# Performance work log

Measured on AMD Instinct MI355X. Metric: run time of the kernel, lower is better.

The kernel has to match this reference:

```python
import jax, jax.numpy as jnp
import numpy as np

B, H, L, E, MODES = 32, 8, 4096, 64, 64


def setup_inputs() -> dict:
    key = jax.random.key(0)
    kx, kw, ki = jax.random.split(key, 3)
    x = jax.random.normal(kx, (B, H, L, E), dtype=jnp.float32)
    # nn.Parameter(torch.randn(E, E, modes, 2) / sqrt(E))
    weights = jax.random.normal(kw, (E, E, MODES, 2), dtype=jnp.float32) / np.sqrt(E)
    # register_buffer: sorted random permutation of [0, seq_len//2) truncated to modes (unique)
    index = jnp.sort(jax.random.permutation(ki, L // 2)[:MODES]).astype(jnp.int64)
    return {"x": x, "weights": weights, "index": index}


def reference(x, weights, index):
    # x: [B, H, L, E]
    Bs, Hs, Ls, Es = x.shape
    xt = jnp.swapaxes(x, -1, -2)                 # [B, H, E, L]
    x_ft = jnp.fft.rfft(xt, axis=-1)             # [B, H, E, L//2+1] complex64
    w_c = weights[..., 0] + 1j * weights[..., 1]  # [E, E, modes] complex
    sel = x_ft[..., index]                       # gather selected modes: [B, H, E, modes]
    out_sel = jnp.einsum('bhei,eoi->bhoi', sel, w_c)  # [B, H, E_out, modes]
    out_ft = jnp.zeros_like(x_ft).at[..., index].set(out_sel)  # scatter into zero spectrum
    y = jnp.fft.irfft(out_ft, n=Ls, axis=-1)     # [B, H, E, L]
    return jnp.swapaxes(y, -1, -2)               # [B, H, L, E]
```

## Files before the change

kernel.cpp:

```cpp
#include <hip/hip_runtime.h>
#include <hip/hip_bf16.h>
#include <math.h>

#define LTOT   4096
#define EDIM   64
#define NMODES 64
#define BH     256
#define TWO_PI 6.28318530717958647692f

typedef float f32x4 __attribute__((ext_vector_type(4)));
typedef short s16x8 __attribute__((ext_vector_type(8)));

__device__ inline unsigned short f2bf(float f) {
    unsigned u = __builtin_bit_cast(unsigned, f);
    u += 0x7fff + ((u >> 16) & 1);
    return (unsigned short)(u >> 16);
}
__device__ inline unsigned packbf(float lo, float hi) {
    float2 t; t.x = lo; t.y = hi;
    __hip_bfloat162 h = __float22bfloat162_rn(t);
    unsigned r;
    __builtin_memcpy(&r, &h, 4);
    return r;
}
__device__ inline float bf2f(unsigned lo16) {
    return __builtin_bit_cast(float, lo16 << 16);
}

__global__ __launch_bounds__(256) void k_tables(const int* __restrict__ index,
                                                const float* __restrict__ w,
                                                unsigned short* __restrict__ Tm,
                                                unsigned short* __restrict__ Tt,
                                                unsigned* __restrict__ wt) {
    int b = blockIdx.x, t = threadIdx.x;
    if (b < 64) {
        int k = b, f = index[k];
        for (int l = t; l < LTOT; l += 256) {
            int m = (f * l) & (LTOT - 1);
            float th = (float)m * (TWO_PI / (float)LTOT);
            float s, c; sincosf(th, &s, &c);
            Tm[(size_t)(2 * k) * LTOT + l]     = f2bf(c);
            Tm[(size_t)(2 * k + 1) * LTOT + l] = f2bf(-s);
        }
    } else if (b < 64 + 1024) {
        int l = (b - 64) * 4 + (t >> 6);
        int k = t & 63, f = index[k];
        int m = (f * l) & (LTOT - 1);
        float th = (float)m * (TWO_PI / (float)LTOT);
        float s, c; sincosf(th, &s, &c);
        ((unsigned*)Tt)[l * 64 + k] = packbf(c, s);
    } else {
        int i = (b - 1088) * 256 + t;
        float2 v = ((const float2*)w)[i];
        wt[i] = packbf(v.x, v.y);
    }
}

__global__ __launch_bounds__(256, 5) void k_stage1(const float* __restrict__ x,
                                                   const unsigned short* __restrict__ Tm,
                                                   float* __restrict__ Xp) {
    int bh = blockIdx.x >> 2, part = blockIdx.x & 3;
    const float* xb = x + ((size_t)bh * LTOT + part * 1024) * EDIM;
    __shared__ unsigned xT[64 * 68];

    int t = threadIdx.x;
    int q = t & 15, lp0 = t >> 4;
    int lane = t & 63, w = t >> 6;
    int r = lane & 15, kb8 = lane >> 4;
    int es = w & 1, ms = w >> 1;
    unsigned swzW = ((unsigned)(q & 7)) << 2;

    f32x4 acc[2][4];
    #pragma unroll
    for (int i = 0; i < 2; ++i)
        #pragma unroll
        for (int n = 0; n < 4; ++n) acc[i][n] = (f32x4)0.f;

    float4 xn[8];
    {
        #pragma unroll
        for (int p = 0; p < 4; ++p) {
            const float* bp = xb + (size_t)(2 * (lp0 + p * 16)) * EDIM + 4 * q;
            xn[2 * p]     = *(const float4*)bp;
            xn[2 * p + 1] = *(const float4*)(bp + EDIM);
        }
    }
    for (int t8 = 0; t8 < 8; ++t8) {
        #pragma unroll
        for (int p = 0; p < 4; ++p) {
            float A0[4] = {xn[2*p].x, xn[2*p].y, xn[2*p].z, xn[2*p].w};
            float A1[4] = {xn[2*p+1].x, xn[2*p+1].y, xn[2*p+1].z, xn[2*p+1].w};
            #pragma unroll
            for (int j = 0; j < 4; ++j)
                xT[(4 * q + j) * 68 + (((unsigned)(lp0 + p * 16)) ^ swzW)] = packbf(A0[j], A1[j]);
        }
        __syncthreads();
        if (t8 < 7) {
            const float* tb = xb + (size_t)((t8 + 1) * 128) * EDIM;
            #pragma unroll
            for (int p = 0; p < 4; ++p) {
                const float* bp = tb + (size_t)(2 * (lp0 + p * 16)) * EDIM + 4 * q;
                xn[2 * p]     = *(const float4*)bp;
                xn[2 * p + 1] = *(const float4*)(bp + EDIM);
            }
        }
        #pragma unroll
        for (int kk = 0; kk < 4; ++kk) {
            s16x8 af[2];
            #pragma unroll
            for (int sub = 0; sub < 2; ++sub) {
                int row = es * 32 + sub * 16 + r;
                unsigned swz = (((unsigned)sub) << 4) + (((unsigned)(r >> 2)) << 2);
                af[sub] = *(const s16x8*)(xT + row * 68 + (((unsigned)(kk * 16 + kb8 * 4)) ^ swz));
            }
            #pragma unroll
            for (int ns = 0; ns < 4; ++ns) {
                int m = ms * 64 + ns * 16 + r;
                s16x8 bf = *(const s16x8*)(Tm + (size_t)m * LTOT + part * 1024 + t8 * 128 + kk * 32 + kb8 * 8);
                acc[0][ns] = __builtin_amdgcn_mfma_f32_16x16x32_bf16(af[0], bf, acc[0][ns], 0, 0, 0);
                acc[1][ns] = __builtin_amdgcn_mfma_f32_16x16x32_bf16(af[1], bf, acc[1][ns], 0, 0, 0);
            }
        }
        __syncthreads();
    }

    float* Xb = Xp + ((size_t)part * BH + bh) * (64 * 128);
    #pragma unroll
    for (int sub = 0; sub < 2; ++sub)
        #pragma unroll
        for (int ns = 0; ns < 4; ++ns)
            #pragma unroll
            for (int g = 0; g < 4; ++g)
                Xb[(es * 32 + sub * 16 + kb8 * 4 + g) * 128 + ms * 64 + ns * 16 + r] = acc[sub][ns][g];
}

__global__ __launch_bounds__(512) void k_stage2(const float* __restrict__ Xp,
                                                const unsigned* __restrict__ wtab,
                                                const int* __restrict__ index,
                                                unsigned* __restrict__ ABo) {
    int bh = blockIdx.x;
    __shared__ float XsR[64 * 68];
    __shared__ float XsI[64 * 68];
    int t = threadIdx.x;

    #pragma unroll
    for (int i = 0; i < 4; ++i) {
        int idx = t + i * 512;
        f32x4 v = (f32x4)0.f;
        #pragma unroll
        for (int p = 0; p < 4; ++p)
            v += ((const f32x4*)(Xp + ((size_t)p * BH + bh) * 8192))[idx];
        int e = idx >> 5, k0 = (idx & 31) * 2;
        XsR[e * 68 + k0]     = v.x;
        XsI[e * 68 + k0]     = v.y;
        XsR[e * 68 + k0 + 1] = v.z;
        XsI[e * 68 + k0 + 1] = v.w;
    }
    __syncthreads();

    int k = t & 63, og = t >> 6;
    int f = index[k];
    float cc = (f == 0 ? 1.0f : 2.0f) / (float)LTOT;
    int o0 = og * 8;
    float aR[8] = {}, aI[8] = {};
    for (int e = 0; e < 64; ++e) {
        float xr = XsR[e * 68 + k];
        float xi = XsI[e * 68 + k];
        #pragma unroll
        for (int oi = 0; oi < 8; ++oi) {
            unsigned wv = wtab[((size_t)(e * 64 + o0 + oi)) * 64 + k];
            float wr = bf2f(wv & 0xffffu);
            float wi = bf2f(wv >> 16);
            aR[oi] += xr * wr - xi * wi;
            aI[oi] += xr * wi + xi * wr;
        }
    }
    #pragma unroll
    for (int oi = 0; oi < 8; ++oi) {
        float im = (f == 0) ? 0.0f : -cc * aI[oi];
        ABo[((size_t)bh * 64 + o0 + oi) * 64 + k] = packbf(cc * aR[oi], im);
    }
}

#define S3P16 136
__global__ __launch_bounds__(256, 4) void k_stage3(const unsigned short* __restrict__ Tt,
                                                   const unsigned* __restrict__ ABo,
                                                   float* __restrict__ y) {
    int bh = blockIdx.x >> 2, qtr = blockIdx.x & 3;
    __shared__ unsigned short ABl[64 * S3P16];
    int t = threadIdx.x;
    int lane = t & 63, wave = t >> 6;
    int r = lane & 15, kb8 = lane >> 4;

    {
        const unsigned* src = ABo + (size_t)bh * 4096;
        unsigned* dst = (unsigned*)ABl;
        #pragma unroll
        for (int i = 0; i < 16; ++i) {
            int idx = t + i * 256;
            int o = idx >> 6, c = idx & 63;
            dst[o * (S3P16 / 2) + c] = src[idx];
        }
    }
    __syncthreads();

    s16x8 afr[4][4];
    #pragma unroll
    for (int es = 0; es < 4; ++es)
        #pragma unroll
        for (int ks = 0; ks < 4; ++ks)
            afr[es][ks] = *(const s16x8*)(ABl + (es * 16 + r) * S3P16 + ks * 32 + kb8 * 8);

    for (int it = 0; it < 16; ++it) {
        int ltile = qtr * 1024 + it * 64 + wave * 16;
        s16x8 btf[4];
        #pragma unroll
        for (int ks = 0; ks < 4; ++ks)
            btf[ks] = *(const s16x8*)(Tt + (size_t)(ltile + r) * 128 + ks * 32 + kb8 * 8);
        f32x4 acc[4];
        #pragma unroll
        for (int es = 0; es < 4; ++es) acc[es] = (f32x4)0.f;
        #pragma unroll
        for (int ks = 0; ks < 4; ++ks)
            #pragma unroll
            for (int es = 0; es < 4; ++es)
                acc[es] = __builtin_amdgcn_mfma_f32_16x16x32_bf16(afr[es][ks], btf[ks], acc[es], 0, 0, 0);
        float* yb = y + ((size_t)bh * LTOT + ltile + r) * EDIM;
        #pragma unroll
        for (int es = 0; es < 4; ++es)
            *(f32x4*)(yb + es * 16 + kb8 * 4) = acc[es];
    }
}

extern "C" void kernel_launch(void* const* d_in, const int* in_sizes, int n_in,
                              void* d_out, int out_size, void* d_ws, size_t ws_size,
                              hipStream_t stream) {
    const float* x     = (const float*)d_in[0];
    const float* wgt   = (const float*)d_in[1];
    const int*   index = (const int*)d_in[2];
    float* y  = (float*)d_out;
    float* ws = (float*)d_ws;

    unsigned short* Tm = (unsigned short*)ws;
    unsigned short* Tt = (unsigned short*)(ws + 262144);
    unsigned*       wt = (unsigned*)(ws + 524288);
    float*          Xp = ws + 786432;
    unsigned*       ABo = (unsigned*)(ws + 9175040);

    hipLaunchKernelGGL(k_tables, dim3(2112),   dim3(256), 0, stream, index, wgt, Tm, Tt, wt);
    hipLaunchKernelGGL(k_stage1, dim3(BH * 4), dim3(256), 0, stream, x, Tm, Xp);
    hipLaunchKernelGGL(k_stage2, dim3(BH),     dim3(512), 0, stream, Xp, wt, index, ABo);
    hipLaunchKernelGGL(k_stage3, dim3(BH * 4), dim3(256), 0, stream, Tt, ABo, y);
}
```

Measured before the change: 226.2 us.

## Store stage-1 partial spectra as bf16, transpose weight table, widen stage 2

```diff
diff --git a/kernel.cpp b/kernel.cpp
--- a/kernel.cpp
+++ b/kernel.cpp
@@ -31,34 +31,38 @@
                                                 const float* __restrict__ w,
                                                 unsigned short* __restrict__ Tm,
                                                 unsigned short* __restrict__ Tt,
-                                                unsigned* __restrict__ wt) {
+                                                unsigned* __restrict__ wt2) {
     int b = blockIdx.x, t = threadIdx.x;
-    if (b < 64) {
-        int k = b, f = index[k];
-        for (int l = t; l < LTOT; l += 256) {
+    if (b < 256) {
+        int k = b >> 2, f = index[k];
+        int lq = b & 3;
+        #pragma unroll
+        for (int i = 0; i < 4; ++i) {
+            int l = lq * 1024 + i * 256 + t;
             int m = (f * l) & (LTOT - 1);
             float th = (float)m * (TWO_PI / (float)LTOT);
             float s, c; sincosf(th, &s, &c);
             Tm[(size_t)(2 * k) * LTOT + l]     = f2bf(c);
             Tm[(size_t)(2 * k + 1) * LTOT + l] = f2bf(-s);
         }
-    } else if (b < 64 + 1024) {
-        int l = (b - 64) * 4 + (t >> 6);
+    } else if (b < 256 + 1024) {
+        int l = (b - 256) * 4 + (t >> 6);
         int k = t & 63, f = index[k];
         int m = (f * l) & (LTOT - 1);
         float th = (float)m * (TWO_PI / (float)LTOT);
         float s, c; sincosf(th, &s, &c);
         ((unsigned*)Tt)[l * 64 + k] = packbf(c, s);
     } else {
-        int i = (b - 1088) * 256 + t;
+        int i = (b - 1280) * 256 + t;
+        int e = i >> 12, o = (i >> 6) & 63, k = i & 63;
         float2 v = ((const float2*)w)[i];
-        wt[i] = packbf(v.x, v.y);
+        wt2[((size_t)(e * 64 + k)) * 64 + o] = packbf(v.x, v.y);
     }
 }
 
 __global__ __launch_bounds__(256, 5) void k_stage1(const float* __restrict__ x,
                                                    const unsigned short* __restrict__ Tm,
-                                                   float* __restrict__ Xp) {
+                                                   unsigned* __restrict__ XpB) {
     int bh = blockIdx.x >> 2, part = blockIdx.x & 3;
     const float* xb = x + ((size_t)bh * LTOT + part * 1024) * EDIM;
     __shared__ unsigned xT[64 * 68];
@@ -124,20 +128,24 @@
         __syncthreads();
     }
 
-    float* Xb = Xp + ((size_t)part * BH + bh) * (64 * 128);
+    unsigned* Xb = XpB + ((size_t)part * BH + bh) * (128 * 32);
     #pragma unroll
     for (int sub = 0; sub < 2; ++sub)
         #pragma unroll
-        for (int ns = 0; ns < 4; ++ns)
-            #pragma unroll
-            for (int g = 0; g < 4; ++g)
-                Xb[(es * 32 + sub * 16 + kb8 * 4 + g) * 128 + ms * 64 + ns * 16 + r] = acc[sub][ns][g];
-}
-
-__global__ __launch_bounds__(512) void k_stage2(const float* __restrict__ Xp,
-                                                const unsigned* __restrict__ wtab,
-                                                const int* __restrict__ index,
-                                                unsigned* __restrict__ ABo) {
+        for (int ns = 0; ns < 4; ++ns) {
+            int m   = ms * 64 + ns * 16 + r;
+            int eu0 = es * 16 + sub * 8 + kb8 * 2;
+            uint2 pv;
+            pv.x = packbf(acc[sub][ns][0], acc[sub][ns][1]);
+            pv.y = packbf(acc[sub][ns][2], acc[sub][ns][3]);
+            *(uint2*)(Xb + m * 32 + eu0) = pv;
+        }
+}
+
+__global__ __launch_bounds__(1024) void k_stage2(const unsigned* __restrict__ XpB,
+                                                 const unsigned* __restrict__ wt2,
+                                                 const int* __restrict__ index,
+                                                 unsigned* __restrict__ ABo) {
     int bh = blockIdx.x;
     __shared__ float XsR[64 * 68];
     __shared__ float XsI[64 * 68];
@@ -145,38 +153,43 @@
 
     #pragma unroll
     for (int i = 0; i < 4; ++i) {
-        int idx = t + i * 512;
-        f32x4 v = (f32x4)0.f;
-        #pragma unroll
-        for (int p = 0; p < 4; ++p)
-            v += ((const f32x4*)(Xp + ((size_t)p * BH + bh) * 8192))[idx];
-        int e = idx >> 5, k0 = (idx & 31) * 2;
-        XsR[e * 68 + k0]     = v.x;
-        XsI[e * 68 + k0]     = v.y;
-        XsR[e * 68 + k0 + 1] = v.z;
-        XsI[e * 68 + k0 + 1] = v.w;
+        int idx = t + i * 1024;
+        float lo = 0.f, hi = 0.f;
+        #pragma unroll
+        for (int p = 0; p < 4; ++p) {
+            unsigned v = XpB[((size_t)p * BH + bh) * 4096 + idx];
+            lo += bf2f(v & 0xffffu);
+            hi += bf2f(v >> 16);
+        }
+        int m = idx >> 5, eu = idx & 31;
+        float* plane = (m & 1) ? XsI : XsR;
+        int k = m >> 1;
+        plane[(2 * eu) * 68 + k]     = lo;
+        plane[(2 * eu + 1) * 68 + k] = hi;
     }
     __syncthreads();
 
     int k = t & 63, og = t >> 6;
     int f = index[k];
     float cc = (f == 0 ? 1.0f : 2.0f) / (float)LTOT;
-    int o0 = og * 8;
-    float aR[8] = {}, aI[8] = {};
+    int o0 = og * 4;
+    float aR[4] = {}, aI[4] = {};
+    #pragma unroll 4
     for (int e = 0; e < 64; ++e) {
         float xr = XsR[e * 68 + k];
         float xi = XsI[e * 68 + k];
-        #pragma unroll
-        for (int oi = 0; oi < 8; ++oi) {
-            unsigned wv = wtab[((size_t)(e * 64 + o0 + oi)) * 64 + k];
-            float wr = bf2f(wv & 0xffffu);
-            float wi = bf2f(wv >> 16);
+        uint4 wv = *(const uint4*)&wt2[((size_t)(e * 64 + k)) * 64 + o0];
+        unsigned wa[4] = {wv.x, wv.y, wv.z, wv.w};
+        #pragma unroll
+        for (int oi = 0; oi < 4; ++oi) {
+            float wr = bf2f(wa[oi] & 0xffffu);
+            float wi = bf2f(wa[oi] >> 16);
             aR[oi] += xr * wr - xi * wi;
             aI[oi] += xr * wi + xi * wr;
         }
     }
     #pragma unroll
-    for (int oi = 0; oi < 8; ++oi) {
+    for (int oi = 0; oi < 4; ++oi) {
         float im = (f == 0) ? 0.0f : -cc * aI[oi];
         ABo[((size_t)bh * 64 + o0 + oi) * 64 + k] = packbf(cc * aR[oi], im);
     }
@@ -241,14 +254,14 @@
     float* y  = (float*)d_out;
     float* ws = (float*)d_ws;
 
-    unsigned short* Tm = (unsigned short*)ws;
-    unsigned short* Tt = (unsigned short*)(ws + 262144);
-    unsigned*       wt = (unsigned*)(ws + 524288);
-    float*          Xp = ws + 786432;
-    unsigned*       ABo = (unsigned*)(ws + 9175040);
-
-    hipLaunchKernelGGL(k_tables, dim3(2112),   dim3(256), 0, stream, index, wgt, Tm, Tt, wt);
-    hipLaunchKernelGGL(k_stage1, dim3(BH * 4), dim3(256), 0, stream, x, Tm, Xp);
-    hipLaunchKernelGGL(k_stage2, dim3(BH),     dim3(512), 0, stream, Xp, wt, index, ABo);
-    hipLaunchKernelGGL(k_stage3, dim3(BH * 4), dim3(256), 0, stream, Tt, ABo, y);
-}
+    unsigned short* Tm  = (unsigned short*)ws;
+    unsigned short* Tt  = (unsigned short*)(ws + 262144);
+    unsigned*       wt2 = (unsigned*)(ws + 524288);
+    unsigned*       XpB = (unsigned*)(ws + 786432);
+    unsigned*       ABo = (unsigned*)(ws + 4980736);
+
+    hipLaunchKernelGGL(k_tables, dim3(2304),   dim3(256),  0, stream, index, wgt, Tm, Tt, wt2);
+    hipLaunchKernelGGL(k_stage1, dim3(BH * 4), dim3(256),  0, stream, x, Tm, XpB);
+    hipLaunchKernelGGL(k_stage2, dim3(BH),     dim3(1024), 0, stream, XpB, wt2, index, ABo);
+    hipLaunchKernelGGL(k_stage3, dim3(BH * 4), dim3(256),  0, stream, Tt, ABo, y);
+}
```

Measured after the change: 243.8 us. 7.8% more time.
